# Optimization experiments

Hardware: AMD Instinct MI355X
Metric: run time of the kernel (lower is better)

Reference implementation:

```python
import jax, jax.numpy as jnp
import numpy as np

G = 64          # groups of the dynamic conv
EPS = 1e-5      # instance-norm epsilon


def setup_inputs() -> dict:
    key = jax.random.key(0)
    ks = jax.random.split(key, 12)
    B, Cin, Cout, S = 16, 512, 256, 512   # batch, in_ch, out_ch, style_dim
    H = W = 32
    cg = Cin // G                          # channels per group (= 8)

    def n(k, shape, scale=0.05):
        return jax.random.normal(k, shape, dtype=jnp.float32) * scale

    return {
        "x": jax.random.normal(ks[0], (B, Cin, H, W), dtype=jnp.float32),
        "w": jax.random.normal(ks[1], (B, S, 3, 3), dtype=jnp.float32),
        # KernelPredictor params
        "kp_sw": n(ks[2], (Cin * cg, S, 3, 3)),   # spatial (depthwise) kernel predictor conv
        "kp_sb": n(ks[3], (Cin * cg,)),
        "kp_pw": n(ks[4], (Cin * cg, S)),          # pointwise kernel predictor (1x1 on pooled style)
        "kp_pb": n(ks[5], (Cin * cg,)),
        "kp_bw": n(ks[6], (Cin, S)),               # bias predictor
        "kp_bb": n(ks[7], (Cin,)),
        # decoder conv stack (convs=2, last changes channels)
        "dec_w1": n(ks[8], (Cin, Cin, 3, 3)),
        "dec_b1": n(ks[9], (Cin,)),
        "dec_w2": n(ks[10], (Cout, Cin, 3, 3)),
        "dec_b2": n(ks[11], (Cout,)),
    }


def _conv(x, w, b=None, groups=1, pad=((1, 1), (1, 1))):
    y = jax.lax.conv_general_dilated(
        x, w, (1, 1), pad, feature_group_count=groups,
        dimension_numbers=("NCHW", "OIHW", "NCHW"))
    if b is not None:
        y = y + b[None, :, None, None]
    return y


def _instance_norm(x):
    m = x.mean(axis=(2, 3), keepdims=True)
    v = x.var(axis=(2, 3), keepdims=True)
    return (x - m) * jax.lax.rsqrt(v + EPS)


def reference(x, w, kp_sw, kp_sb, kp_pw, kp_pb, kp_bw, kp_bb,
              dec_w1, dec_b1, dec_w2, dec_b2):
    B, C, H, W_ = x.shape
    cg = C // G
    # ---- KernelPredictor ----
    # spatial branch: reflect-padded 3x3 conv over the 3x3 style map -> per-sample grouped spatial kernels
    w_pad = jnp.pad(w, ((0, 0), (0, 0), (1, 1), (1, 1)), mode="reflect")
    dw = _conv(w_pad, kp_sw, kp_sb, pad=((0, 0), (0, 0)))      # [B, C*cg, 3, 3]
    dw = dw.reshape(B, C, cg, 3, 3)                             # [B, out, in/g, kh, kw]
    # pointwise + bias branches: global avg pool then 1x1 conv (== matmul)
    pooled = w.mean(axis=(2, 3))                                # [B, S]
    pw = (pooled @ kp_pw.T + kp_pb).reshape(B, G, cg, cg)       # [B, g, out_pg, in_pg]
    bias = pooled @ kp_bw.T + kp_bb                             # [B, C]
    # ---- AdaConv2D: instance-norm, per-sample grouped spatial conv, grouped pointwise conv + bias ----
    xn = _instance_norm(x)
    xp = jnp.pad(xn, ((0, 0), (0, 0), (1, 1), (1, 1)), mode="reflect")

    def per_sample(xi, ki):
        return _conv(xi[None], ki, groups=G, pad=((0, 0), (0, 0)))[0]

    y = jax.vmap(per_sample)(xp, dw)                            # [B, C, H, W]
    yg = y.reshape(B, G, cg, H, W_)
    y = jnp.einsum("bgoi,bgihw->bgohw", pw, yg).reshape(B, C, H, W_)
    y = y + bias[:, :, None, None]
    # ---- decoder conv stack + nearest upsample ----
    y = jax.nn.relu(_conv(y, dec_w1, dec_b1))
    y = jax.nn.relu(_conv(y, dec_w2, dec_b2))
    y = jnp.repeat(jnp.repeat(y, 2, axis=2), 2, axis=3)         # 32x32 -> 64x64 nearest
    return y
```

## Files before the change

### kernel.cpp

```cpp
#include <hip/hip_runtime.h>

using short8 = __attribute__((ext_vector_type(8))) short;
using f32x4  = __attribute__((ext_vector_type(4))) float;

__device__ __forceinline__ unsigned short f2b(float f){
  unsigned int u = __float_as_uint(f);
  u = u + 0x7fffu + ((u >> 16) & 1u);
  return (unsigned short)(u >> 16);
}
__device__ __forceinline__ float b2f(unsigned short s){
  return __uint_as_float(((unsigned int)s) << 16);
}

__device__ __forceinline__ void gll16(const void* g, void* l){
  __builtin_amdgcn_global_load_lds(
      (const __attribute__((address_space(1))) unsigned int*)g,
      (__attribute__((address_space(3))) unsigned int*)l, 16, 0, 0);
}
__device__ __forceinline__ void vm_wait4(){ asm volatile("s_waitcnt vmcnt(4)" ::: "memory"); }
__device__ __forceinline__ void vm_wait0(){ asm volatile("s_waitcnt vmcnt(0)" ::: "memory"); }

__global__ __launch_bounds__(256) void k_prepwt(const float* __restrict__ w,
    unsigned short* __restrict__ A, float* __restrict__ pooled,
    const float* __restrict__ w1, const float* __restrict__ w2,
    unsigned short* __restrict__ d1, unsigned short* __restrict__ d2){
  int bid = blockIdx.x;
  if(bid >= 176){
    __shared__ float ld[4608];
    int co = bid - 176;
    const float* src = (co < 512) ? (w1 + (size_t)co * 4608) : (w2 + (size_t)(co - 512) * 4608);
    unsigned short* dst = (co < 512) ? (d1 + (size_t)co * 4608) : (d2 + (size_t)(co - 512) * 4608);
    for(int i = threadIdx.x; i < 4608; i += 256) ld[i] = src[i];
    __syncthreads();
    for(int i = threadIdx.x; i < 4608; i += 256){
      int q = i >> 9, cin = i & 511;
      dst[i] = f2b(ld[cin * 9 + q]);
    }
    return;
  }
  if(bid >= 144){
    int i = (bid - 144) * 256 + threadIdx.x;
    const float* p = w + (size_t)i * 9;
    float s = 0.f;
    #pragma unroll
    for(int j = 0; j < 9; j++) s += p[j];
    pooled[i] = s * (1.f / 9.f);
    return;
  }
  int row = bid;
  int pos = row >> 4, b = row & 15;
  int oh = pos / 3, ow = pos % 3;
  for(int k = threadIdx.x; k < 4608; k += 256){
    int cin = k / 9, q = k - cin * 9;
    int kh = q / 3, kw = q - kh * 3;
    int ih = oh + kh - 1, iw = ow + kw - 1;
    ih = ih < 0 ? -ih : (ih > 2 ? 4 - ih : ih);
    iw = iw < 0 ? -iw : (iw > 2 ? 4 - iw : iw);
    float v = w[((size_t)(b * 512 + cin) * 3 + ih) * 3 + iw];
    A[(size_t)row * 4608 + k] = f2b(v);
  }
}

__global__ __launch_bounds__(256) void k_pwgemm(const unsigned short* __restrict__ Aim,
    const float* __restrict__ kp_sw, float* __restrict__ part,
    const float* __restrict__ pooled,
    const float* __restrict__ kp_pw, const float* __restrict__ kp_pb,
    const float* __restrict__ kp_bw, const float* __restrict__ kp_bb,
    float* __restrict__ pw, float* __restrict__ bias){
  __shared__ unsigned short Al[144 * 72];
  __shared__ unsigned short Bl[64 * 72];
  int bid = blockIdx.x;
  int tid = threadIdx.x;
  int lane = tid & 63, wv = tid >> 6;
  if(bid >= 768){
    int wid = ((bid - 768) * 256 + tid) >> 6;
    const float* row;
    float bv;
    if(wid < 4096){ row = kp_pw + (size_t)wid * 512; bv = kp_pb[wid]; }
    else          { row = kp_bw + (size_t)(wid - 4096) * 512; bv = kp_bb[wid - 4096]; }
    float r[8];
    #pragma unroll
    for(int i = 0; i < 8; i++) r[i] = row[lane + 64 * i];
    for(int b = 0; b < 16; b++){
      float s = 0.f;
      #pragma unroll
      for(int i = 0; i < 8; i++) s += r[i] * pooled[b * 512 + lane + 64 * i];
      #pragma unroll
      for(int o = 32; o >= 1; o >>= 1) s += __shfl_xor(s, o, 64);
      if(lane == 0){
        if(wid < 4096) pw[b * 4096 + wid] = s + bv;
        else           bias[b * 512 + (wid - 4096)] = s + bv;
      }
    }
    return;
  }
  int n0 = (bid & 63) * 64;
  int kz = bid >> 6;
  f32x4 acc[9] = {};
  for(int ks = kz * 6; ks < kz * 6 + 6; ks++){
    int kb = ks * 64;
    for(int c = tid; c < 1152; c += 256){
      int m = c >> 3, kc = c & 7;
      *(int4*)&Al[m * 72 + kc * 8] = *(const int4*)(Aim + (size_t)m * 4608 + kb + kc * 8);
    }
    for(int c = tid; c < 512; c += 256){
      int n = c >> 3, kc = c & 7;
      const float4* src = (const float4*)(kp_sw + (size_t)(n0 + n) * 4608 + kb + kc * 8);
      float4 v0 = src[0], v1 = src[1];
      unsigned short tmp[8];
      tmp[0]=f2b(v0.x); tmp[1]=f2b(v0.y); tmp[2]=f2b(v0.z); tmp[3]=f2b(v0.w);
      tmp[4]=f2b(v1.x); tmp[5]=f2b(v1.y); tmp[6]=f2b(v1.z); tmp[7]=f2b(v1.w);
      *(int4*)&Bl[n * 72 + kc * 8] = *(int4*)tmp;
    }
    __syncthreads();
    int r16 = lane & 15, khalf = lane >> 4;
    #pragma unroll
    for(int kk = 0; kk < 2; kk++){
      int ko = kk * 32 + khalf * 8;
      short8 bf = *(const short8*)&Bl[(wv * 16 + r16) * 72 + ko];
      #pragma unroll
      for(int mf = 0; mf < 9; mf++){
        short8 af = *(const short8*)&Al[(mf * 16 + r16) * 72 + ko];
        acc[mf] = __builtin_amdgcn_mfma_f32_16x16x32_bf16(af, bf, acc[mf], 0, 0, 0);
      }
    }
    __syncthreads();
  }
  int r16 = lane & 15, rgrp = lane >> 4;
  int n = n0 + wv * 16 + r16;
  #pragma unroll
  for(int mf = 0; mf < 9; mf++){
    #pragma unroll
    for(int r = 0; r < 4; r++){
      int m = mf * 16 + rgrp * 4 + r;
      part[((size_t)kz * 144 + m) * 4096 + n] = acc[mf][r];
    }
  }
}

__global__ __launch_bounds__(256) void k_red(const float* __restrict__ part,
    const float* __restrict__ kp_sb, float* __restrict__ dw){
  int i = blockIdx.x * 256 + threadIdx.x;
  int m = i >> 12, n = i & 4095;
  float s = kp_sb[n];
  #pragma unroll
  for(int kz = 0; kz < 12; kz++) s += part[((size_t)kz * 144 + m) * 4096 + n];
  int q = m >> 4, b = m & 15;
  dw[((size_t)b * 4096 + n) * 9 + q] = s;
}

__global__ __launch_bounds__(256) void k_ada(const float* __restrict__ x,
    const float* __restrict__ dwb, const float* __restrict__ pwb,
    const float* __restrict__ biasb, unsigned short* __restrict__ y0p,
    unsigned short* __restrict__ y1p){
  int bg = blockIdx.x;
  if(bg >= 1024){
    int i = (bg - 1024) * 256 + threadIdx.x;
    int b = i / 8448, rem = i - b * 8448;
    int e = rem >> 6, ch8 = rem & 63;
    int hh, ww;
    if(e < 34){ hh = 0; ww = e; }
    else if(e < 68){ hh = 33; ww = e - 34; }
    else if(e < 100){ hh = e - 68 + 1; ww = 0; }
    else { hh = e - 100 + 1; ww = 33; }
    int4 z = {0, 0, 0, 0};
    *(int4*)&y1p[((size_t)(b * 34 + hh) * 34 + ww) * 512 + ch8 * 8] = z;
    return;
  }
  __shared__ float xn[8][1156];
  __shared__ float dwl[576];
  __shared__ float pwl[64];
  __shared__ float bl[8];
  __shared__ float red0[4][8], red1[4][8];
  __shared__ float ms[8], rs[8];
  int b = bg >> 6, g = bg & 63;
  int tid = threadIdx.x;
  int lane = tid & 63, wv = tid >> 6;
  for(int i = tid; i < 576; i += 256) dwl[i] = dwb[((size_t)b * 4096 + g * 64) * 9 + i];
  if(tid < 64) pwl[tid] = pwb[b * 4096 + g * 64 + tid];
  if(tid < 8)  bl[tid]  = biasb[b * 512 + g * 8 + tid];
  if(tid < 132){
    int e = tid, hh, ww;
    if(e < 34){ hh = 0; ww = e; }
    else if(e < 68){ hh = 33; ww = e - 34; }
    else if(e < 100){ hh = e - 68 + 1; ww = 0; }
    else { hh = e - 100 + 1; ww = 33; }
    int4 z = {0, 0, 0, 0};
    *(int4*)&y0p[((size_t)(b * 34 + hh) * 34 + ww) * 512 + g * 8] = z;
  }
  const float* xb = x + ((size_t)(b * 512 + g * 8)) * 1024;
  int h4 = tid >> 3, w4 = (tid & 7) * 4;
  float s[8], s2[8];
  #pragma unroll
  for(int ci = 0; ci < 8; ci++){
    float4 v = *(const float4*)(xb + ci * 1024 + tid * 4);
    float* dst = &xn[ci][(h4 + 1) * 34 + w4 + 1];
    dst[0] = v.x; dst[1] = v.y; dst[2] = v.z; dst[3] = v.w;
    s[ci]  = v.x + v.y + v.z + v.w;
    s2[ci] = v.x * v.x + v.y * v.y + v.z * v.z + v.w * v.w;
  }
  #pragma unroll
  for(int ci = 0; ci < 8; ci++){
    #pragma unroll
    for(int o = 32; o >= 1; o >>= 1){
      s[ci]  += __shfl_xor(s[ci],  o, 64);
      s2[ci] += __shfl_xor(s2[ci], o, 64);
    }
  }
  if(lane == 0){
    #pragma unroll
    for(int ci = 0; ci < 8; ci++){ red0[wv][ci] = s[ci]; red1[wv][ci] = s2[ci]; }
  }
  __syncthreads();
  if(tid < 8){
    float S  = red0[0][tid] + red0[1][tid] + red0[2][tid] + red0[3][tid];
    float S2 = red1[0][tid] + red1[1][tid] + red1[2][tid] + red1[3][tid];
    float m = S * (1.f / 1024.f);
    ms[tid] = m;
    rs[tid] = rsqrtf(S2 * (1.f / 1024.f) - m * m + 1e-5f);
  }
  __syncthreads();
  #pragma unroll
  for(int ci = 0; ci < 8; ci++){
    float m = ms[ci], r = rs[ci];
    float* p = &xn[ci][(h4 + 1) * 34 + w4 + 1];
    #pragma unroll
    for(int j = 0; j < 4; j++) p[j] = (p[j] - m) * r;
  }
  __syncthreads();
  for(int idx = tid; idx < 1056; idx += 256){
    int ci = idx / 132, e = idx - ci * 132;
    int hh, ww;
    if(e < 34){ hh = 0; ww = e; }
    else if(e < 68){ hh = 33; ww = e - 34; }
    else if(e < 100){ hh = e - 68 + 1; ww = 0; }
    else { hh = e - 100 + 1; ww = 33; }
    int h = hh - 1, w2 = ww - 1;
    h  = h  < 0 ? 1 : (h  > 31 ? 30 : h);
    w2 = w2 < 0 ? 1 : (w2 > 31 ? 30 : w2);
    xn[ci][hh * 34 + ww] = xn[ci][(h + 1) * 34 + (w2 + 1)];
  }
  __syncthreads();
  float acc[4][8] = {};
  #pragma unroll
  for(int i = 0; i < 8; i++){
    #pragma unroll
    for(int q = 0; q < 9; q++){
      int kh = q / 3, kw = q - kh * 3;
      float dvs[8];
      #pragma unroll
      for(int o = 0; o < 8; o++) dvs[o] = dwl[(o * 8 + i) * 9 + q];
      #pragma unroll
      for(int pp = 0; pp < 4; pp++){
        int p = pp * 256 + tid; int h = p >> 5, w = p & 31;
        float v = xn[i][(h + kh) * 34 + (w + kw)];
        #pragma unroll
        for(int o = 0; o < 8; o++) acc[pp][o] += v * dvs[o];
      }
    }
  }
  #pragma unroll
  for(int pp = 0; pp < 4; pp++){
    int p = pp * 256 + tid; int h = p >> 5, w = p & 31;
    unsigned short pack[8];
    #pragma unroll
    for(int o = 0; o < 8; o++){
      float sv = bl[o];
      #pragma unroll
      for(int i2 = 0; i2 < 8; i2++) sv += pwl[o * 8 + i2] * acc[pp][i2];
      pack[o] = f2b(sv);
    }
    *(int4*)&y0p[((size_t)(b * 34 + h + 1) * 34 + (w + 1)) * 512 + g * 8] = *(int4*)pack;
  }
}

template<int FUSE_UP>
__global__ __launch_bounds__(512, 4) void k_convP(const unsigned short* __restrict__ inp,
    const unsigned short* __restrict__ wt, const float* __restrict__ bias,
    unsigned short* __restrict__ outp, float* __restrict__ outf){
  __shared__ __align__(16) char smraw[65536];
  unsigned short (*Al)[128 * 64] = (unsigned short(*)[128 * 64])smraw;
  unsigned short (*Bl)[128 * 64] = (unsigned short(*)[128 * 64])(smraw + 32768);
  float* red = (float*)smraw;
  int tid = threadIdx.x;
  int mt = blockIdx.x;
  int n0 = blockIdx.y * 128;
  int b = mt >> 3, h0 = (mt & 7) * 4;
  int lane = tid & 63, wv = tid >> 6;
  int khv = wv >> 2, wsub = wv & 3;
  int wm = (wsub >> 1) * 64, wn = (wsub & 1) * 64;
  f32x4 acc[4][4] = {};
  const size_t bbase = (size_t)b * 34 * 34 * 512;

  int kc = tid & 7;
  int m0 = tid >> 3, m1 = (tid + 512) >> 3;
  int colA0 = kc ^ (m0 & 7), colA1 = kc ^ (m1 & 7);
  int mh0 = m0 >> 5, mw0 = m0 & 31;
  int mh1 = m1 >> 5, mw1 = m1 & 31;
  int ldsO0 = (tid & ~63) * 8;
  int ldsO1 = ldsO0 + 512 * 8;
  const unsigned short* a0base = inp + bbase + colA0 * 8;
  const unsigned short* a1base = inp + bbase + colA1 * 8;
  const unsigned short* b0base = wt + (size_t)(n0 + m0) * 4608 + colA0 * 8;
  const unsigned short* b1base = wt + (size_t)(n0 + m1) * 4608 + colA1 * 8;
  int r16 = lane & 15, khalf = lane >> 4;
  int sc8 = ((khv * 4 + khalf) ^ (r16 & 7)) * 8;

#define STAGE(T, BUF) { \
    int q_ = (T) >> 3, cb_ = ((T) & 7) * 64; \
    int kh_ = q_ / 3, kw_ = q_ - kh_ * 3; \
    gll16(a0base + (size_t)((h0 + mh0 + kh_) * 34 + mw0 + kw_) * 512 + cb_, &Al[BUF][ldsO0]); \
    gll16(a1base + (size_t)((h0 + mh1 + kh_) * 34 + mw1 + kw_) * 512 + cb_, &Al[BUF][ldsO1]); \
    gll16(b0base + (size_t)q_ * 512 + cb_, &Bl[BUF][ldsO0]); \
    gll16(b1base + (size_t)q_ * 512 + cb_, &Bl[BUF][ldsO1]); }

#define COMPUTE(BUF) { \
    short8 af[4], bf[4]; \
    _Pragma("unroll") for(int i = 0; i < 4; i++) af[i] = *(const short8*)&Al[BUF][(wm + i * 16 + r16) * 64 + sc8]; \
    _Pragma("unroll") for(int i = 0; i < 4; i++) bf[i] = *(const short8*)&Bl[BUF][(wn + i * 16 + r16) * 64 + sc8]; \
    __builtin_amdgcn_s_setprio(1); \
    _Pragma("unroll") for(int mi = 0; mi < 4; mi++) \
      _Pragma("unroll") for(int ni = 0; ni < 4; ni++) \
        acc[mi][ni] = __builtin_amdgcn_mfma_f32_16x16x32_bf16(af[mi], bf[ni], acc[mi][ni], 0, 0, 0); \
    __builtin_amdgcn_s_setprio(0); }

  STAGE(0, 0)
  STAGE(1, 1)
  vm_wait4(); __builtin_amdgcn_s_barrier();
  for(int t = 0; t < 70; t += 2){
    COMPUTE(0)
    __builtin_amdgcn_s_barrier();
    STAGE(t + 2, 0)
    vm_wait4(); __builtin_amdgcn_s_barrier();
    COMPUTE(1)
    __builtin_amdgcn_s_barrier();
    STAGE(t + 3, 1)
    vm_wait4(); __builtin_amdgcn_s_barrier();
  }
  COMPUTE(0)
  vm_wait0(); __builtin_amdgcn_s_barrier();
  COMPUTE(1)
#undef STAGE
#undef COMPUTE

  __syncthreads();
  if(khv == 1){
    float* dst = red + wsub * 4096 + lane * 4;
    #pragma unroll
    for(int mi = 0; mi < 4; mi++)
      #pragma unroll
      for(int ni = 0; ni < 4; ni++)
        *(f32x4*)(dst + (mi * 4 + ni) * 256) = acc[mi][ni];
  }
  __syncthreads();
  if(khv == 0){
    const float* src = red + wsub * 4096 + lane * 4;
    #pragma unroll
    for(int mi = 0; mi < 4; mi++)
      #pragma unroll
      for(int ni = 0; ni < 4; ni++)
        acc[mi][ni] += *(const f32x4*)(src + (mi * 4 + ni) * 256);

    int rgrp = lane >> 4;
    #pragma unroll
    for(int ni = 0; ni < 4; ni++){
      int n = n0 + wn + ni * 16 + r16;
      float bv = bias[n];
      #pragma unroll
      for(int mi = 0; mi < 4; mi++){
        int row0 = wm + mi * 16 + rgrp * 4;
        int h = h0 + (row0 >> 5), w0 = row0 & 31;
        float v[4];
        #pragma unroll
        for(int r = 0; r < 4; r++){
          float t = acc[mi][ni][r] + bv;
          v[r] = t > 0.f ? t : 0.f;
        }
        if(FUSE_UP){
          size_t base = ((size_t)(b * 256 + n) * 64 + 2 * h) * 64 + 2 * w0;
          float4 f0 = make_float4(v[0], v[0], v[1], v[1]);
          float4 f1 = make_float4(v[2], v[2], v[3], v[3]);
          *(float4*)&outf[base]          = f0;
          *(float4*)&outf[base + 4]      = f1;
          *(float4*)&outf[base + 64]     = f0;
          *(float4*)&outf[base + 64 + 4] = f1;
        } else {
          #pragma unroll
          for(int r = 0; r < 4; r++){
            int w = w0 + r;
            outp[((size_t)(b * 34 + h + 1) * 34 + (w + 1)) * 512 + n] = f2b(v[r]);
          }
        }
      }
    }
  }
}

extern "C" void kernel_launch(void* const* d_in, const int* in_sizes, int n_in,
                              void* d_out, int out_size, void* d_ws, size_t ws_size,
                              hipStream_t stream){
  (void)in_sizes; (void)n_in; (void)out_size; (void)ws_size;
  const float* x      = (const float*)d_in[0];
  const float* w      = (const float*)d_in[1];
  const float* kp_sw  = (const float*)d_in[2];
  const float* kp_sb  = (const float*)d_in[3];
  const float* kp_pw  = (const float*)d_in[4];
  const float* kp_pb  = (const float*)d_in[5];
  const float* kp_bw  = (const float*)d_in[6];
  const float* kp_bb  = (const float*)d_in[7];
  const float* dec_w1 = (const float*)d_in[8];
  const float* dec_b1 = (const float*)d_in[9];
  const float* dec_w2 = (const float*)d_in[10];
  const float* dec_b2 = (const float*)d_in[11];
  char* ws = (char*)d_ws;
  float*          pooled = (float*)(ws);
  float*          pw     = (float*)(ws + 32768);
  float*          bias   = (float*)(ws + 294912);
  unsigned short* Aim    = (unsigned short*)(ws + 393216);
  float*          dw     = (float*)(ws + 1720320);
  unsigned short* w1t    = (unsigned short*)(ws + 4079616);
  unsigned short* w2t    = (unsigned short*)(ws + 8798208);
  unsigned short* y0p    = (unsigned short*)(ws + 11157504);
  unsigned short* y1p    = (unsigned short*)(ws + 30097408);
  float*          part   = (float*)(ws + 11157504);

  k_prepwt<<<944,  256, 0, stream>>>(w, Aim, pooled, dec_w1, dec_w2, w1t, w2t);
  k_pwgemm<<<1920, 256, 0, stream>>>(Aim, kp_sw, part, pooled,
                                     kp_pw, kp_pb, kp_bw, kp_bb, pw, bias);
  k_red   <<<2304, 256, 0, stream>>>(part, kp_sb, dw);
  k_ada   <<<1552, 256, 0, stream>>>(x, dw, pw, bias, y0p, y1p);
  k_convP<0><<<dim3(128, 4), 512, 0, stream>>>(y0p, w1t, dec_b1, y1p, nullptr);
  k_convP<1><<<dim3(128, 2), 512, 0, stream>>>(y1p, w2t, dec_b2, nullptr, (float*)d_out);
}
```

Baseline: 219.4 us.

## Fuse split-K reduction into AdaConv, move border zeroing, retile conv2

```diff
diff --git a/kernel.cpp b/kernel.cpp
--- a/kernel.cpp
+++ b/kernel.cpp
@@ -18,6 +18,7 @@
       (__attribute__((address_space(3))) unsigned int*)l, 16, 0, 0);
 }
 __device__ __forceinline__ void vm_wait4(){ asm volatile("s_waitcnt vmcnt(4)" ::: "memory"); }
+__device__ __forceinline__ void vm_wait3(){ asm volatile("s_waitcnt vmcnt(3)" ::: "memory"); }
 __device__ __forceinline__ void vm_wait0(){ asm volatile("s_waitcnt vmcnt(0)" ::: "memory"); }
 
 __global__ __launch_bounds__(256) void k_prepwt(const float* __restrict__ w,
@@ -72,8 +73,8 @@
   int bid = blockIdx.x;
   int tid = threadIdx.x;
   int lane = tid & 63, wv = tid >> 6;
-  if(bid >= 768){
-    int wid = ((bid - 768) * 256 + tid) >> 6;
+  if(bid >= 512){
+    int wid = ((bid - 512) * 256 + tid) >> 6;
     const float* row;
     float bv;
     if(wid < 4096){ row = kp_pw + (size_t)wid * 512; bv = kp_pb[wid]; }
@@ -97,7 +98,7 @@
   int n0 = (bid & 63) * 64;
   int kz = bid >> 6;
   f32x4 acc[9] = {};
-  for(int ks = kz * 6; ks < kz * 6 + 6; ks++){
+  for(int ks = kz * 9; ks < kz * 9 + 9; ks++){
     int kb = ks * 64;
     for(int c = tid; c < 1152; c += 256){
       int m = c >> 3, kc = c & 7;
@@ -138,45 +139,28 @@
   }
 }
 
-__global__ __launch_bounds__(256) void k_red(const float* __restrict__ part,
-    const float* __restrict__ kp_sb, float* __restrict__ dw){
-  int i = blockIdx.x * 256 + threadIdx.x;
-  int m = i >> 12, n = i & 4095;
-  float s = kp_sb[n];
-  #pragma unroll
-  for(int kz = 0; kz < 12; kz++) s += part[((size_t)kz * 144 + m) * 4096 + n];
-  int q = m >> 4, b = m & 15;
-  dw[((size_t)b * 4096 + n) * 9 + q] = s;
-}
-
 __global__ __launch_bounds__(256) void k_ada(const float* __restrict__ x,
-    const float* __restrict__ dwb, const float* __restrict__ pwb,
-    const float* __restrict__ biasb, unsigned short* __restrict__ y0p,
-    unsigned short* __restrict__ y1p){
-  int bg = blockIdx.x;
-  if(bg >= 1024){
-    int i = (bg - 1024) * 256 + threadIdx.x;
-    int b = i / 8448, rem = i - b * 8448;
-    int e = rem >> 6, ch8 = rem & 63;
-    int hh, ww;
-    if(e < 34){ hh = 0; ww = e; }
-    else if(e < 68){ hh = 33; ww = e - 34; }
-    else if(e < 100){ hh = e - 68 + 1; ww = 0; }
-    else { hh = e - 100 + 1; ww = 33; }
-    int4 z = {0, 0, 0, 0};
-    *(int4*)&y1p[((size_t)(b * 34 + hh) * 34 + ww) * 512 + ch8 * 8] = z;
-    return;
-  }
+    const float* __restrict__ part, const float* __restrict__ kp_sb,
+    const float* __restrict__ pwb, const float* __restrict__ biasb,
+    unsigned short* __restrict__ y0p){
   __shared__ float xn[8][1156];
   __shared__ float dwl[576];
   __shared__ float pwl[64];
   __shared__ float bl[8];
   __shared__ float red0[4][8], red1[4][8];
   __shared__ float ms[8], rs[8];
+  int bg = blockIdx.x;
   int b = bg >> 6, g = bg & 63;
   int tid = threadIdx.x;
   int lane = tid & 63, wv = tid >> 6;
-  for(int i = tid; i < 576; i += 256) dwl[i] = dwb[((size_t)b * 4096 + g * 64) * 9 + i];
+  for(int i = tid; i < 576; i += 256){
+    int q = i >> 6, nl = i & 63;
+    float s = kp_sb[g * 64 + nl];
+    #pragma unroll
+    for(int kz = 0; kz < 8; kz++)
+      s += part[((size_t)(kz * 144 + q * 16 + b)) * 4096 + g * 64 + nl];
+    dwl[nl * 9 + q] = s;
+  }
   if(tid < 64) pwl[tid] = pwb[b * 4096 + g * 64 + tid];
   if(tid < 8)  bl[tid]  = biasb[b * 512 + g * 8 + tid];
   if(tid < 132){
@@ -274,15 +258,28 @@
   }
 }
 
-template<int FUSE_UP>
-__global__ __launch_bounds__(512, 4) void k_convP(const unsigned short* __restrict__ inp,
+__global__ __launch_bounds__(512, 4) void k_conv1(const unsigned short* __restrict__ inp,
     const unsigned short* __restrict__ wt, const float* __restrict__ bias,
-    unsigned short* __restrict__ outp, float* __restrict__ outf){
+    unsigned short* __restrict__ outp){
+  int tid = threadIdx.x;
+  if(blockIdx.y == 4){
+    for(int i = blockIdx.x * 512 + tid; i < 135168; i += 65536){
+      int b = i / 8448, rem = i - b * 8448;
+      int e = rem >> 6, ch8 = rem & 63;
+      int hh, ww;
+      if(e < 34){ hh = 0; ww = e; }
+      else if(e < 68){ hh = 33; ww = e - 34; }
+      else if(e < 100){ hh = e - 68 + 1; ww = 0; }
+      else { hh = e - 100 + 1; ww = 33; }
+      int4 z = {0, 0, 0, 0};
+      *(int4*)&outp[((size_t)(b * 34 + hh) * 34 + ww) * 512 + ch8 * 8] = z;
+    }
+    return;
+  }
   __shared__ __align__(16) char smraw[65536];
   unsigned short (*Al)[128 * 64] = (unsigned short(*)[128 * 64])smraw;
   unsigned short (*Bl)[128 * 64] = (unsigned short(*)[128 * 64])(smraw + 32768);
   float* red = (float*)smraw;
-  int tid = threadIdx.x;
   int mt = blockIdx.x;
   int n0 = blockIdx.y * 128;
   int b = mt >> 3, h0 = (mt & 7) * 4;
@@ -360,10 +357,114 @@
       #pragma unroll
       for(int ni = 0; ni < 4; ni++)
         acc[mi][ni] += *(const f32x4*)(src + (mi * 4 + ni) * 256);
-
     int rgrp = lane >> 4;
     #pragma unroll
     for(int ni = 0; ni < 4; ni++){
+      int n = n0 + wn + ni * 16 + r16;
+      float bv = bias[n];
+      #pragma unroll
+      for(int mi = 0; mi < 4; mi++){
+        #pragma unroll
+        for(int r = 0; r < 4; r++){
+          int row = wm + mi * 16 + rgrp * 4 + r;
+          int h = h0 + (row >> 5), w = row & 31;
+          float v = acc[mi][ni][r] + bv;
+          v = v > 0.f ? v : 0.f;
+          outp[((size_t)(b * 34 + h + 1) * 34 + (w + 1)) * 512 + n] = f2b(v);
+        }
+      }
+    }
+  }
+}
+
+__global__ __launch_bounds__(512, 4) void k_conv2up(const unsigned short* __restrict__ inp,
+    const unsigned short* __restrict__ wt, const float* __restrict__ bias,
+    float* __restrict__ outf){
+  __shared__ __align__(16) char smraw[49152];
+  unsigned short (*Al)[128 * 64] = (unsigned short(*)[128 * 64])smraw;
+  unsigned short (*Bl)[64 * 64]  = (unsigned short(*)[64 * 64])(smraw + 32768);
+  float* red = (float*)smraw;
+  int tid = threadIdx.x;
+  int mt = blockIdx.x;
+  int n0 = blockIdx.y * 64;
+  int b = mt >> 3, h0 = (mt & 7) * 4;
+  int lane = tid & 63, wv = tid >> 6;
+  int khv = wv >> 2, wsub = wv & 3;
+  int wm = (wsub >> 1) * 64, wn = (wsub & 1) * 32;
+  f32x4 acc[4][2] = {};
+  const size_t bbase = (size_t)b * 34 * 34 * 512;
+
+  int kc = tid & 7;
+  int m0 = tid >> 3, m1 = (tid + 512) >> 3;
+  int colA0 = kc ^ (m0 & 7), colA1 = kc ^ (m1 & 7);
+  int mh0 = m0 >> 5, mw0 = m0 & 31;
+  int mh1 = m1 >> 5, mw1 = m1 & 31;
+  int nB = tid >> 3;
+  int cB = kc ^ (nB & 7);
+  int ldsO0 = (tid & ~63) * 8;
+  int ldsO1 = ldsO0 + 512 * 8;
+  const unsigned short* a0base = inp + bbase + colA0 * 8;
+  const unsigned short* a1base = inp + bbase + colA1 * 8;
+  const unsigned short* bbse = wt + (size_t)(n0 + nB) * 4608 + cB * 8;
+  int r16 = lane & 15, khalf = lane >> 4;
+  int sc8 = ((khv * 4 + khalf) ^ (r16 & 7)) * 8;
+
+#define STAGE(T, BUF) { \
+    int q_ = (T) >> 3, cb_ = ((T) & 7) * 64; \
+    int kh_ = q_ / 3, kw_ = q_ - kh_ * 3; \
+    gll16(a0base + (size_t)((h0 + mh0 + kh_) * 34 + mw0 + kw_) * 512 + cb_, &Al[BUF][ldsO0]); \
+    gll16(a1base + (size_t)((h0 + mh1 + kh_) * 34 + mw1 + kw_) * 512 + cb_, &Al[BUF][ldsO1]); \
+    gll16(bbse + (size_t)q_ * 512 + cb_, &Bl[BUF][ldsO0]); }
+
+#define COMPUTE(BUF) { \
+    short8 af[4], bf[2]; \
+    _Pragma("unroll") for(int i = 0; i < 4; i++) af[i] = *(const short8*)&Al[BUF][(wm + i * 16 + r16) * 64 + sc8]; \
+    _Pragma("unroll") for(int i = 0; i < 2; i++) bf[i] = *(const short8*)&Bl[BUF][(wn + i * 16 + r16) * 64 + sc8]; \
+    __builtin_amdgcn_s_setprio(1); \
+    _Pragma("unroll") for(int mi = 0; mi < 4; mi++) \
+      _Pragma("unroll") for(int ni = 0; ni < 2; ni++) \
+        acc[mi][ni] = __builtin_amdgcn_mfma_f32_16x16x32_bf16(af[mi], bf[ni], acc[mi][ni], 0, 0, 0); \
+    __builtin_amdgcn_s_setprio(0); }
+
+  STAGE(0, 0)
+  STAGE(1, 1)
+  vm_wait3(); __builtin_amdgcn_s_barrier();
+  for(int t = 0; t < 70; t += 2){
+    COMPUTE(0)
+    __builtin_amdgcn_s_barrier();
+    STAGE(t + 2, 0)
+    vm_wait3(); __builtin_amdgcn_s_barrier();
+    COMPUTE(1)
+    __builtin_amdgcn_s_barrier();
+    STAGE(t + 3, 1)
+    vm_wait3(); __builtin_amdgcn_s_barrier();
+  }
+  COMPUTE(0)
+  vm_wait0(); __builtin_amdgcn_s_barrier();
+  COMPUTE(1)
+#undef STAGE
+#undef COMPUTE
+
+  __syncthreads();
+  if(khv == 1){
+    float* dst = red + wsub * 2048 + lane * 4;
+    #pragma unroll
+    for(int mi = 0; mi < 4; mi++)
+      #pragma unroll
+      for(int ni = 0; ni < 2; ni++)
+        *(f32x4*)(dst + (mi * 2 + ni) * 256) = acc[mi][ni];
+  }
+  __syncthreads();
+  if(khv == 0){
+    const float* src = red + wsub * 2048 + lane * 4;
+    #pragma unroll
+    for(int mi = 0; mi < 4; mi++)
+      #pragma unroll
+      for(int ni = 0; ni < 2; ni++)
+        acc[mi][ni] += *(const f32x4*)(src + (mi * 2 + ni) * 256);
+    int rgrp = lane >> 4;
+    #pragma unroll
+    for(int ni = 0; ni < 2; ni++){
       int n = n0 + wn + ni * 16 + r16;
       float bv = bias[n];
       #pragma unroll
@@ -376,21 +477,13 @@
           float t = acc[mi][ni][r] + bv;
           v[r] = t > 0.f ? t : 0.f;
         }
-        if(FUSE_UP){
-          size_t base = ((size_t)(b * 256 + n) * 64 + 2 * h) * 64 + 2 * w0;
-          float4 f0 = make_float4(v[0], v[0], v[1], v[1]);
-          float4 f1 = make_float4(v[2], v[2], v[3], v[3]);
-          *(float4*)&outf[base]          = f0;
-          *(float4*)&outf[base + 4]      = f1;
-          *(float4*)&outf[base + 64]     = f0;
-          *(float4*)&outf[base + 64 + 4] = f1;
-        } else {
-          #pragma unroll
-          for(int r = 0; r < 4; r++){
-            int w = w0 + r;
-            outp[((size_t)(b * 34 + h + 1) * 34 + (w + 1)) * 512 + n] = f2b(v[r]);
-          }
-        }
+        size_t base = ((size_t)(b * 256 + n) * 64 + 2 * h) * 64 + 2 * w0;
+        float4 f0 = make_float4(v[0], v[0], v[1], v[1]);
+        float4 f1 = make_float4(v[2], v[2], v[3], v[3]);
+        *(float4*)&outf[base]          = f0;
+        *(float4*)&outf[base + 4]      = f1;
+        *(float4*)&outf[base + 64]     = f0;
+        *(float4*)&outf[base + 64 + 4] = f1;
       }
     }
   }
@@ -417,18 +510,16 @@
   float*          pw     = (float*)(ws + 32768);
   float*          bias   = (float*)(ws + 294912);
   unsigned short* Aim    = (unsigned short*)(ws + 393216);
-  float*          dw     = (float*)(ws + 1720320);
   unsigned short* w1t    = (unsigned short*)(ws + 4079616);
   unsigned short* w2t    = (unsigned short*)(ws + 8798208);
   unsigned short* y0p    = (unsigned short*)(ws + 11157504);
   unsigned short* y1p    = (unsigned short*)(ws + 30097408);
-  float*          part   = (float*)(ws + 11157504);
+  float*          part   = (float*)(ws + 30097408);
 
   k_prepwt<<<944,  256, 0, stream>>>(w, Aim, pooled, dec_w1, dec_w2, w1t, w2t);
-  k_pwgemm<<<1920, 256, 0, stream>>>(Aim, kp_sw, part, pooled,
+  k_pwgemm<<<1664, 256, 0, stream>>>(Aim, kp_sw, part, pooled,
                                      kp_pw, kp_pb, kp_bw, kp_bb, pw, bias);
-  k_red   <<<2304, 256, 0, stream>>>(part, kp_sb, dw);
-  k_ada   <<<1552, 256, 0, stream>>>(x, dw, pw, bias, y0p, y1p);
-  k_convP<0><<<dim3(128, 4), 512, 0, stream>>>(y0p, w1t, dec_b1, y1p, nullptr);
-  k_convP<1><<<dim3(128, 2), 512, 0, stream>>>(y1p, w2t, dec_b2, nullptr, (float*)d_out);
-}
+  k_ada   <<<1024, 256, 0, stream>>>(x, part, kp_sb, pw, bias, y0p);
+  k_conv1 <<<dim3(128, 5), 512, 0, stream>>>(y0p, w1t, dec_b1, y1p);
+  k_conv2up<<<dim3(128, 4), 512, 0, stream>>>(y1p, w2t, dec_b2, (float*)d_out);
+}
```

New measurement: 216.3 us, median of 2. Within noise of the previous version (-1.5%).

## Restructure decoder conv with input slab reuse, fuse split-K reduce into ada

Applied to the files above, without the earlier changes.

```diff
diff --git a/kernel.cpp b/kernel.cpp
--- a/kernel.cpp
+++ b/kernel.cpp
@@ -17,7 +17,6 @@
       (const __attribute__((address_space(1))) unsigned int*)g,
       (__attribute__((address_space(3))) unsigned int*)l, 16, 0, 0);
 }
-__device__ __forceinline__ void vm_wait4(){ asm volatile("s_waitcnt vmcnt(4)" ::: "memory"); }
 __device__ __forceinline__ void vm_wait0(){ asm volatile("s_waitcnt vmcnt(0)" ::: "memory"); }
 
 __global__ __launch_bounds__(256) void k_prepwt(const float* __restrict__ w,
@@ -72,8 +71,8 @@
   int bid = blockIdx.x;
   int tid = threadIdx.x;
   int lane = tid & 63, wv = tid >> 6;
-  if(bid >= 768){
-    int wid = ((bid - 768) * 256 + tid) >> 6;
+  if(bid >= 512){
+    int wid = ((bid - 512) * 256 + tid) >> 6;
     const float* row;
     float bv;
     if(wid < 4096){ row = kp_pw + (size_t)wid * 512; bv = kp_pb[wid]; }
@@ -97,7 +96,7 @@
   int n0 = (bid & 63) * 64;
   int kz = bid >> 6;
   f32x4 acc[9] = {};
-  for(int ks = kz * 6; ks < kz * 6 + 6; ks++){
+  for(int ks = kz * 9; ks < kz * 9 + 9; ks++){
     int kb = ks * 64;
     for(int c = tid; c < 1152; c += 256){
       int m = c >> 3, kc = c & 7;
@@ -138,45 +137,28 @@
   }
 }
 
-__global__ __launch_bounds__(256) void k_red(const float* __restrict__ part,
-    const float* __restrict__ kp_sb, float* __restrict__ dw){
-  int i = blockIdx.x * 256 + threadIdx.x;
-  int m = i >> 12, n = i & 4095;
-  float s = kp_sb[n];
-  #pragma unroll
-  for(int kz = 0; kz < 12; kz++) s += part[((size_t)kz * 144 + m) * 4096 + n];
-  int q = m >> 4, b = m & 15;
-  dw[((size_t)b * 4096 + n) * 9 + q] = s;
-}
-
 __global__ __launch_bounds__(256) void k_ada(const float* __restrict__ x,
-    const float* __restrict__ dwb, const float* __restrict__ pwb,
-    const float* __restrict__ biasb, unsigned short* __restrict__ y0p,
-    unsigned short* __restrict__ y1p){
-  int bg = blockIdx.x;
-  if(bg >= 1024){
-    int i = (bg - 1024) * 256 + threadIdx.x;
-    int b = i / 8448, rem = i - b * 8448;
-    int e = rem >> 6, ch8 = rem & 63;
-    int hh, ww;
-    if(e < 34){ hh = 0; ww = e; }
-    else if(e < 68){ hh = 33; ww = e - 34; }
-    else if(e < 100){ hh = e - 68 + 1; ww = 0; }
-    else { hh = e - 100 + 1; ww = 33; }
-    int4 z = {0, 0, 0, 0};
-    *(int4*)&y1p[((size_t)(b * 34 + hh) * 34 + ww) * 512 + ch8 * 8] = z;
-    return;
-  }
+    const float* __restrict__ part, const float* __restrict__ kp_sb,
+    const float* __restrict__ pwb, const float* __restrict__ biasb,
+    unsigned short* __restrict__ y0p){
   __shared__ float xn[8][1156];
   __shared__ float dwl[576];
   __shared__ float pwl[64];
   __shared__ float bl[8];
   __shared__ float red0[4][8], red1[4][8];
   __shared__ float ms[8], rs[8];
+  int bg = blockIdx.x;
   int b = bg >> 6, g = bg & 63;
   int tid = threadIdx.x;
   int lane = tid & 63, wv = tid >> 6;
-  for(int i = tid; i < 576; i += 256) dwl[i] = dwb[((size_t)b * 4096 + g * 64) * 9 + i];
+  for(int i = tid; i < 576; i += 256){
+    int q = i >> 6, nl = i & 63;
+    float s = kp_sb[g * 64 + nl];
+    #pragma unroll
+    for(int kz = 0; kz < 8; kz++)
+      s += part[((size_t)(kz * 144 + q * 16 + b)) * 4096 + g * 64 + nl];
+    dwl[nl * 9 + q] = s;
+  }
   if(tid < 64) pwl[tid] = pwb[b * 4096 + g * 64 + tid];
   if(tid < 8)  bl[tid]  = biasb[b * 512 + g * 8 + tid];
   if(tid < 132){
@@ -274,125 +256,169 @@
   }
 }
 
-template<int FUSE_UP>
-__global__ __launch_bounds__(512, 4) void k_convP(const unsigned short* __restrict__ inp,
+template<int BN, int NB, int FUSE_UP>
+__global__ __launch_bounds__(512, 4) void k_convS(const unsigned short* __restrict__ inp,
     const unsigned short* __restrict__ wt, const float* __restrict__ bias,
     unsigned short* __restrict__ outp, float* __restrict__ outf){
-  __shared__ __align__(16) char smraw[65536];
-  unsigned short (*Al)[128 * 64] = (unsigned short(*)[128 * 64])smraw;
-  unsigned short (*Bl)[128 * 64] = (unsigned short(*)[128 * 64])(smraw + 32768);
+  int tid = threadIdx.x;
+  if(FUSE_UP == 0 && blockIdx.y == 4){
+    for(int i = blockIdx.x * 512 + tid; i < 135168; i += 65536){
+      int b = i / 8448, rem = i - b * 8448;
+      int e = rem >> 6, ch8 = rem & 63;
+      int hh, ww;
+      if(e < 34){ hh = 0; ww = e; }
+      else if(e < 68){ hh = 33; ww = e - 34; }
+      else if(e < 100){ hh = e - 68 + 1; ww = 0; }
+      else { hh = e - 100 + 1; ww = 33; }
+      int4 z = {0, 0, 0, 0};
+      *(int4*)&outp[((size_t)(b * 34 + hh) * 34 + ww) * 512 + ch8 * 8] = z;
+    }
+    return;
+  }
+  constexpr int NF = BN / 32;
+  __shared__ __align__(16) char smraw[26624 + 2 * BN * 128];
+  unsigned short* slab = (unsigned short*)smraw;
   float* red = (float*)smraw;
-  int tid = threadIdx.x;
   int mt = blockIdx.x;
-  int n0 = blockIdx.y * 128;
+  int n0 = blockIdx.y * BN;
   int b = mt >> 3, h0 = (mt & 7) * 4;
   int lane = tid & 63, wv = tid >> 6;
   int khv = wv >> 2, wsub = wv & 3;
-  int wm = (wsub >> 1) * 64, wn = (wsub & 1) * 64;
-  f32x4 acc[4][4] = {};
+  int wm = (wsub >> 1) * 64, wn = (wsub & 1) * (BN / 2);
+  f32x4 acc[4][NF] = {};
   const size_t bbase = (size_t)b * 34 * 34 * 512;
 
-  int kc = tid & 7;
-  int m0 = tid >> 3, m1 = (tid + 512) >> 3;
-  int colA0 = kc ^ (m0 & 7), colA1 = kc ^ (m1 & 7);
-  int mh0 = m0 >> 5, mw0 = m0 & 31;
-  int mh1 = m1 >> 5, mw1 = m1 & 31;
-  int ldsO0 = (tid & ~63) * 8;
-  int ldsO1 = ldsO0 + 512 * 8;
-  const unsigned short* a0base = inp + bbase + colA0 * 8;
-  const unsigned short* a1base = inp + bbase + colA1 * 8;
-  const unsigned short* b0base = wt + (size_t)(n0 + m0) * 4608 + colA0 * 8;
-  const unsigned short* b1base = wt + (size_t)(n0 + m1) * 4608 + colA1 * 8;
+  const unsigned short* sA[4];
+  #pragma unroll
+  for(int j = 0; j < 4; j++){
+    int c = tid + 512 * j;
+    int cc = (c < 1632) ? c : 0;
+    int pix = cc >> 3, c8 = cc & 7;
+    int pr = pix / 34, pc = pix - pr * 34;
+    sA[j] = inp + bbase + ((size_t)(h0 + pr) * 34 + pc) * 512 + (c8 ^ (pix & 7)) * 8;
+  }
+  int ldsA = (tid & ~63) * 8;
+  int kcB = tid & 7;
+  int nB0 = tid >> 3,            nB1 = (tid + 512) >> 3;
+  int cB0 = kcB ^ (nB0 & 7),     cB1 = kcB ^ (nB1 & 7);
+  const unsigned short* sB0 = wt + (size_t)(n0 + nB0) * 4608 + cB0 * 8;
+  const unsigned short* sB1 = wt + (size_t)(n0 + nB1) * 4608 + cB1 * 8;
   int r16 = lane & 15, khalf = lane >> 4;
-  int sc8 = ((khv * 4 + khalf) ^ (r16 & 7)) * 8;
-
-#define STAGE(T, BUF) { \
-    int q_ = (T) >> 3, cb_ = ((T) & 7) * 64; \
-    int kh_ = q_ / 3, kw_ = q_ - kh_ * 3; \
-    gll16(a0base + (size_t)((h0 + mh0 + kh_) * 34 + mw0 + kw_) * 512 + cb_, &Al[BUF][ldsO0]); \
-    gll16(a1base + (size_t)((h0 + mh1 + kh_) * 34 + mw1 + kw_) * 512 + cb_, &Al[BUF][ldsO1]); \
-    gll16(b0base + (size_t)q_ * 512 + cb_, &Bl[BUF][ldsO0]); \
-    gll16(b1base + (size_t)q_ * 512 + cb_, &Bl[BUF][ldsO1]); }
-
-#define COMPUTE(BUF) { \
-    short8 af[4], bf[4]; \
-    _Pragma("unroll") for(int i = 0; i < 4; i++) af[i] = *(const short8*)&Al[BUF][(wm + i * 16 + r16) * 64 + sc8]; \
-    _Pragma("unroll") for(int i = 0; i < 4; i++) bf[i] = *(const short8*)&Bl[BUF][(wn + i * 16 + r16) * 64 + sc8]; \
+  int sK = khv * 4 + khalf;
+  int p0[4];
+  #pragma unroll
+  for(int mi = 0; mi < 4; mi++){
+    int m = wm + mi * 16 + r16;
+    p0[mi] = (m >> 5) * 34 + (m & 31);
+  }
+
+#define VMWAITN { if(NB == 2) asm volatile("s_waitcnt vmcnt(2)" ::: "memory"); \
+                  else        asm volatile("s_waitcnt vmcnt(1)" ::: "memory"); }
+#define STAGE_SLAB(CB) { \
+    gll16(sA[0] + (CB) * 64, &slab[ldsA]); \
+    gll16(sA[1] + (CB) * 64, &slab[ldsA + 512 * 8]); \
+    gll16(sA[2] + (CB) * 64, &slab[ldsA + 1024 * 8]); \
+    if(tid < 128) gll16(sA[3] + (CB) * 64, &slab[ldsA + 1536 * 8]); }
+#define STAGE_B(Q, CB, BUF) { \
+    unsigned short* Bb = (unsigned short*)(smraw + 26624 + (BUF) * (BN * 128)); \
+    gll16(sB0 + (size_t)(Q) * 512 + (CB) * 64, &Bb[ldsA]); \
+    if(NB == 2) gll16(sB1 + (size_t)(Q) * 512 + (CB) * 64, &Bb[ldsA + 512 * 8]); }
+#define COMPUTE(KH, KW, BUF) { \
+    const unsigned short* Bb = (const unsigned short*)(smraw + 26624 + (BUF) * (BN * 128)); \
+    short8 af[4], bf[NF]; \
+    _Pragma("unroll") for(int mi = 0; mi < 4; mi++){ \
+      int pix = p0[mi] + (KH) * 34 + (KW); \
+      af[mi] = *(const short8*)&slab[pix * 64 + (sK ^ (pix & 7)) * 8]; } \
+    _Pragma("unroll") for(int ni = 0; ni < NF; ni++) \
+      bf[ni] = *(const short8*)&Bb[(wn + ni * 16 + r16) * 64 + (sK ^ (r16 & 7)) * 8]; \
     __builtin_amdgcn_s_setprio(1); \
     _Pragma("unroll") for(int mi = 0; mi < 4; mi++) \
-      _Pragma("unroll") for(int ni = 0; ni < 4; ni++) \
+      _Pragma("unroll") for(int ni = 0; ni < NF; ni++) \
         acc[mi][ni] = __builtin_amdgcn_mfma_f32_16x16x32_bf16(af[mi], bf[ni], acc[mi][ni], 0, 0, 0); \
     __builtin_amdgcn_s_setprio(0); }
 
-  STAGE(0, 0)
-  STAGE(1, 1)
-  vm_wait4(); __builtin_amdgcn_s_barrier();
-  for(int t = 0; t < 70; t += 2){
-    COMPUTE(0)
+  STAGE_SLAB(0)
+  STAGE_B(0, 0, 0)
+  STAGE_B(1, 0, 1)
+  VMWAITN __builtin_amdgcn_s_barrier();
+  for(int cb = 0; cb < 8; cb++){
+    #pragma unroll
+    for(int q = 0; q < 7; q++){
+      COMPUTE(q / 3, q % 3, q & 1)
+      __builtin_amdgcn_s_barrier();
+      STAGE_B(q + 2, cb, q & 1)
+      VMWAITN __builtin_amdgcn_s_barrier();
+    }
+    COMPUTE(2, 1, 1)
     __builtin_amdgcn_s_barrier();
-    STAGE(t + 2, 0)
-    vm_wait4(); __builtin_amdgcn_s_barrier();
-    COMPUTE(1)
+    vm_wait0(); __builtin_amdgcn_s_barrier();
+    COMPUTE(2, 2, 0)
     __builtin_amdgcn_s_barrier();
-    STAGE(t + 3, 1)
-    vm_wait4(); __builtin_amdgcn_s_barrier();
-  }
-  COMPUTE(0)
-  vm_wait0(); __builtin_amdgcn_s_barrier();
-  COMPUTE(1)
-#undef STAGE
+    if(cb < 7){
+      STAGE_SLAB(cb + 1)
+      STAGE_B(0, cb + 1, 0)
+      STAGE_B(1, cb + 1, 1)
+      VMWAITN __builtin_amdgcn_s_barrier();
+    }
+  }
+#undef VMWAITN
+#undef STAGE_SLAB
+#undef STAGE_B
 #undef COMPUTE
 
   __syncthreads();
-  if(khv == 1){
-    float* dst = red + wsub * 4096 + lane * 4;
-    #pragma unroll
-    for(int mi = 0; mi < 4; mi++)
-      #pragma unroll
-      for(int ni = 0; ni < 4; ni++)
-        *(f32x4*)(dst + (mi * 4 + ni) * 256) = acc[mi][ni];
-  }
-  __syncthreads();
-  if(khv == 0){
-    const float* src = red + wsub * 4096 + lane * 4;
-    #pragma unroll
-    for(int mi = 0; mi < 4; mi++)
-      #pragma unroll
-      for(int ni = 0; ni < 4; ni++)
-        acc[mi][ni] += *(const f32x4*)(src + (mi * 4 + ni) * 256);
-
-    int rgrp = lane >> 4;
-    #pragma unroll
-    for(int ni = 0; ni < 4; ni++){
-      int n = n0 + wn + ni * 16 + r16;
-      float bv = bias[n];
-      #pragma unroll
-      for(int mi = 0; mi < 4; mi++){
-        int row0 = wm + mi * 16 + rgrp * 4;
-        int h = h0 + (row0 >> 5), w0 = row0 & 31;
-        float v[4];
+  int rgrp = lane >> 4;
+  #pragma unroll
+  for(int g = 0; g < 2; g++){
+    if(khv == 1 && (wsub >> 1) == g){
+      float* dst = red + (wsub & 1) * (NF * 1024) + lane * 4;
+      #pragma unroll
+      for(int mi = 0; mi < 4; mi++)
         #pragma unroll
-        for(int r = 0; r < 4; r++){
-          float t = acc[mi][ni][r] + bv;
-          v[r] = t > 0.f ? t : 0.f;
-        }
-        if(FUSE_UP){
-          size_t base = ((size_t)(b * 256 + n) * 64 + 2 * h) * 64 + 2 * w0;
-          float4 f0 = make_float4(v[0], v[0], v[1], v[1]);
-          float4 f1 = make_float4(v[2], v[2], v[3], v[3]);
-          *(float4*)&outf[base]          = f0;
-          *(float4*)&outf[base + 4]      = f1;
-          *(float4*)&outf[base + 64]     = f0;
-          *(float4*)&outf[base + 64 + 4] = f1;
-        } else {
+        for(int ni = 0; ni < NF; ni++)
+          *(f32x4*)(dst + (mi * NF + ni) * 256) = acc[mi][ni];
+    }
+    __syncthreads();
+    if(khv == 0 && (wsub >> 1) == g){
+      const float* src = red + (wsub & 1) * (NF * 1024) + lane * 4;
+      #pragma unroll
+      for(int mi = 0; mi < 4; mi++)
+        #pragma unroll
+        for(int ni = 0; ni < NF; ni++)
+          acc[mi][ni] += *(const f32x4*)(src + (mi * NF + ni) * 256);
+      #pragma unroll
+      for(int ni = 0; ni < NF; ni++){
+        int n = n0 + wn + ni * 16 + r16;
+        float bv = bias[n];
+        #pragma unroll
+        for(int mi = 0; mi < 4; mi++){
+          int row0 = wm + mi * 16 + rgrp * 4;
+          int h = h0 + (row0 >> 5), w0 = row0 & 31;
+          float v[4];
           #pragma unroll
           for(int r = 0; r < 4; r++){
-            int w = w0 + r;
-            outp[((size_t)(b * 34 + h + 1) * 34 + (w + 1)) * 512 + n] = f2b(v[r]);
+            float t = acc[mi][ni][r] + bv;
+            v[r] = t > 0.f ? t : 0.f;
+          }
+          if(FUSE_UP){
+            size_t base = ((size_t)(b * 256 + n) * 64 + 2 * h) * 64 + 2 * w0;
+            float4 f0 = make_float4(v[0], v[0], v[1], v[1]);
+            float4 f1 = make_float4(v[2], v[2], v[3], v[3]);
+            *(float4*)&outf[base]          = f0;
+            *(float4*)&outf[base + 4]      = f1;
+            *(float4*)&outf[base + 64]     = f0;
+            *(float4*)&outf[base + 64 + 4] = f1;
+          } else {
+            #pragma unroll
+            for(int r = 0; r < 4; r++){
+              int w = w0 + r;
+              outp[((size_t)(b * 34 + h + 1) * 34 + (w + 1)) * 512 + n] = f2b(v[r]);
+            }
           }
         }
       }
     }
+    __syncthreads();
   }
 }
 
@@ -417,18 +443,16 @@
   float*          pw     = (float*)(ws + 32768);
   float*          bias   = (float*)(ws + 294912);
   unsigned short* Aim    = (unsigned short*)(ws + 393216);
-  float*          dw     = (float*)(ws + 1720320);
   unsigned short* w1t    = (unsigned short*)(ws + 4079616);
   unsigned short* w2t    = (unsigned short*)(ws + 8798208);
   unsigned short* y0p    = (unsigned short*)(ws + 11157504);
   unsigned short* y1p    = (unsigned short*)(ws + 30097408);
-  float*          part   = (float*)(ws + 11157504);
+  float*          part   = (float*)(ws + 30097408);
 
   k_prepwt<<<944,  256, 0, stream>>>(w, Aim, pooled, dec_w1, dec_w2, w1t, w2t);
-  k_pwgemm<<<1920, 256, 0, stream>>>(Aim, kp_sw, part, pooled,
+  k_pwgemm<<<1664, 256, 0, stream>>>(Aim, kp_sw, part, pooled,
                                      kp_pw, kp_pb, kp_bw, kp_bb, pw, bias);
-  k_red   <<<2304, 256, 0, stream>>>(part, kp_sb, dw);
-  k_ada   <<<1552, 256, 0, stream>>>(x, dw, pw, bias, y0p, y1p);
-  k_convP<0><<<dim3(128, 4), 512, 0, stream>>>(y0p, w1t, dec_b1, y1p, nullptr);
-  k_convP<1><<<dim3(128, 2), 512, 0, stream>>>(y1p, w2t, dec_b2, nullptr, (float*)d_out);
-}
+  k_ada   <<<1024, 256, 0, stream>>>(x, part, kp_sb, pw, bias, y0p);
+  k_convS<128, 2, 0><<<dim3(128, 5), 512, 0, stream>>>(y0p, w1t, dec_b1, y1p, nullptr);
+  k_convS<64,  1, 1><<<dim3(128, 4), 512, 0, stream>>>(y1p, w2t, dec_b2, nullptr, (float*)d_out);
+}
```

Result: slower. 237.7 us (+8.3%).
